# Kernel optimization log

Hardware: AMD Instinct MI355X
Metric: run time of the kernel (lower is better)

The kernel has to match this reference:

```python
import jax, jax.numpy as jnp
import numpy as np

HEADS = 16
DIM_HEAD = 64
SCALE = DIM_HEAD ** -0.5
MASK_VALUE = -jnp.finfo(jnp.float32).max


def setup_inputs() -> dict:
    key = jax.random.key(0)
    ks = jax.random.split(key, 6)
    b, n, dim = 2, 2048, 1024
    mem_len = 2048
    inner = HEADS * DIM_HEAD  # 1024
    return {
        "x": jax.random.normal(ks[0], (b, n, dim), jnp.float32),
        "mem_k": jax.random.normal(ks[1], (b, mem_len, inner), jnp.float32),
        "mem_v": jax.random.normal(ks[2], (b, mem_len, inner), jnp.float32),
        "pos_bias": jax.random.normal(ks[3], (HEADS, n, mem_len + n), jnp.float32) * 0.02,
        "Wq": jax.random.normal(ks[4], (dim, inner), jnp.float32) * (dim ** -0.5),
        "Wkv": jax.random.normal(ks[5], (dim, 2 * inner), jnp.float32) * (dim ** -0.5),
    }


def reference(x, mem_k, mem_v, pos_bias, Wq, Wkv):
    b, n, _ = x.shape
    # projections (note: original module returns before applying to_out)
    q = (x @ Wq) * SCALE                      # [b, n, h*d]
    k, v = jnp.split(x @ Wkv, 2, axis=-1)     # each [b, n, h*d]
    k = jnp.concatenate((mem_k, k), axis=1)   # [b, j, h*d]
    v = jnp.concatenate((mem_v, v), axis=1)

    def split_heads(t):
        return t.reshape(t.shape[0], t.shape[1], HEADS, DIM_HEAD).transpose(0, 2, 1, 3)

    q, k, v = map(split_heads, (q, k, v))     # [b, h, i/j, d]
    sim = jnp.einsum('bhid,bhjd->bhij', q, k)
    sim = sim + pos_bias[None]                # broadcast over batch
    i, j = sim.shape[-2:]
    # causal mask: triu with offset j - i + 1 is masked out
    causal_mask = jnp.triu(jnp.ones((i, j), dtype=bool), k=j - i + 1)
    sim = jnp.where(causal_mask[None, None], MASK_VALUE, sim)
    attn = jax.nn.softmax(sim, axis=-1)
    out = jnp.einsum('bhij,bhjd->bhid', attn, v)     # [b, h, i, d]
    out = out.transpose(0, 2, 1, 3).reshape(b, n, HEADS * DIM_HEAD)
    return out
```

## Files before the change

kernel.cpp:

```cpp
#include <hip/hip_runtime.h>
#include <hip/hip_bf16.h>
#include <cstdint>

#define B_     2
#define N_     2048
#define DIM_   1024
#define H_     16
#define DH_    64
#define MEM_   2048
#define JT_    4096
#define INNER_ 1024
#define SCALE_ 0.125f

typedef float f32x4 __attribute__((ext_vector_type(4)));
typedef short s16x8 __attribute__((ext_vector_type(8)));
typedef short s16x4 __attribute__((ext_vector_type(4)));

__device__ __forceinline__ short bf16_of(float f) {
    __hip_bfloat16 h = __float2bfloat16(f);
    return *(short*)&h;
}

__device__ __forceinline__ void gload16(const void* g, short* l) {
    __builtin_amdgcn_global_load_lds(
        (const __attribute__((address_space(1))) unsigned int*)g,
        (__attribute__((address_space(3))) unsigned int*)l, 16, 0, 0);
}

__global__ __launch_bounds__(256) void cast_x(
    const float* __restrict__ x, short* __restrict__ xb)
{
    const int total4 = B_ * N_ * DIM_ / 4;
    for (int idx = blockIdx.x * blockDim.x + threadIdx.x; idx < total4;
         idx += gridDim.x * blockDim.x) {
        float4 v = ((const float4*)x)[idx];
        s16x4 o;
        o[0] = bf16_of(v.x); o[1] = bf16_of(v.y);
        o[2] = bf16_of(v.z); o[3] = bf16_of(v.w);
        *(s16x4*)&xb[idx * 4] = o;
    }
}

__global__ __launch_bounds__(256) void cast_w(
    const float* __restrict__ Wq, const float* __restrict__ Wkv,
    short* __restrict__ Wt)
{
    const int kt = blockIdx.x;
    const int nt = blockIdx.y;
    __shared__ float tile[64][65];
    const int t = threadIdx.x;
    const int r = t >> 2, s4 = (t & 3) * 16;

    const int n0 = nt * 64;
    const float* src;
    int ldn, nc0;
    if (n0 < 1024) { src = Wq;  ldn = 1024; nc0 = n0; }
    else           { src = Wkv; ldn = 2048; nc0 = n0 - 1024; }
    const float scale = (n0 < 1024) ? SCALE_ : 1.0f;

#pragma unroll
    for (int kq = 0; kq < 4; ++kq) {
        float4 v = *(const float4*)&src[(size_t)(kt * 64 + r) * ldn + nc0 + s4 + kq * 4];
        tile[s4 + kq * 4 + 0][r] = v.x;
        tile[s4 + kq * 4 + 1][r] = v.y;
        tile[s4 + kq * 4 + 2][r] = v.z;
        tile[s4 + kq * 4 + 3][r] = v.w;
    }
    __syncthreads();
    short ov[16];
#pragma unroll
    for (int e = 0; e < 16; ++e) ov[e] = bf16_of(tile[r][s4 + e] * scale);
    short* dst = &Wt[(size_t)(n0 + r) * 1024 + kt * 64 + s4];
    *(s16x8*)&dst[0] = *(s16x8*)&ov[0];
    *(s16x8*)&dst[8] = *(s16x8*)&ov[8];
}

#define PLDC 152

__global__ __launch_bounds__(256) void mfma_proj(
    const short* __restrict__ Wt, const short* __restrict__ xb,
    short* __restrict__ qbuf, short* __restrict__ kbuf, short* __restrict__ vtbuf)
{
    const int bc = blockIdx.x;
    const int bi = blockIdx.y;
    const int tid = threadIdx.x;
    const int w = tid >> 6, lane = tid & 63, g = lane >> 4, li = lane & 15;
    const int wr = w >> 1, wc = w & 1;

    __shared__ short smem[128 * PLDC];
    short* A_lds = smem;
    short* B_lds = smem + 8192;

    f32x4 acc[4][4];
#pragma unroll
    for (int m = 0; m < 4; ++m)
#pragma unroll
        for (int n = 0; n < 4; ++n) acc[m][n] = f32x4{0.f, 0.f, 0.f, 0.f};

    const size_t arow0 = (size_t)bc * 128;
    const size_t brow0 = (size_t)bi * 128;

    for (int t = 0; t < 16; ++t) {
        __syncthreads();
#pragma unroll
        for (int u = 0; u < 4; ++u) {
            const int c = (w * 4 + u) * 64 + lane;
            const int row = c >> 3, q = c & 7;
            const int qs = q ^ (row & 7);
            gload16(&Wt[(arow0 + row) * 1024 + t * 64 + qs * 8],
                    &A_lds[(w * 4 + u) * 512 + lane * 8]);
            gload16(&xb[(brow0 + row) * 1024 + t * 64 + qs * 8],
                    &B_lds[(w * 4 + u) * 512 + lane * 8]);
        }
        __syncthreads();
#pragma unroll
        for (int kc = 0; kc < 2; ++kc) {
            s16x8 af[4], bf[4];
#pragma unroll
            for (int mt = 0; mt < 4; ++mt) {
                const int row = wr * 64 + mt * 16 + li;
                af[mt] = *(const s16x8*)&A_lds[row * 64 + ((kc * 4 + g) ^ (row & 7)) * 8];
            }
#pragma unroll
            for (int nt = 0; nt < 4; ++nt) {
                const int row = wc * 64 + nt * 16 + li;
                bf[nt] = *(const s16x8*)&B_lds[row * 64 + ((kc * 4 + g) ^ (row & 7)) * 8];
            }
#pragma unroll
            for (int mt = 0; mt < 4; ++mt)
#pragma unroll
                for (int nt = 0; nt < 4; ++nt)
                    acc[mt][nt] = __builtin_amdgcn_mfma_f32_16x16x32_bf16(af[mt], bf[nt], acc[mt][nt], 0, 0, 0);
        }
    }

    __syncthreads();
    const int c0 = bc * 128;
    const int i0g = bi * 128;
    const int b = i0g >> 11;
    const int ii0 = i0g & 2047;

    if (c0 < 2048) {
#pragma unroll
        for (int mt = 0; mt < 4; ++mt)
#pragma unroll
            for (int nt = 0; nt < 4; ++nt) {
                const int i_l = wc * 64 + nt * 16 + li;
                const int c_l = wr * 64 + mt * 16 + g * 4;
                s16x4 v4;
                v4[0] = bf16_of(acc[mt][nt][0]);
                v4[1] = bf16_of(acc[mt][nt][1]);
                v4[2] = bf16_of(acc[mt][nt][2]);
                v4[3] = bf16_of(acc[mt][nt][3]);
                *(s16x4*)&smem[i_l * PLDC + c_l] = v4;
            }
        __syncthreads();
        const bool isq = (c0 < 1024);
#pragma unroll
        for (int u = 0; u < 8; ++u) {
            const int ch = tid + u * 256;
            const int i_l = ch >> 4, seg = ch & 15;
            s16x8 v = *(const s16x8*)&smem[i_l * PLDC + seg * 8];
            const int cg = c0 + seg * 8;
            const int h = (cg >> 6) & 15;
            const int d = cg & 63;
            if (isq)
                *(s16x8*)&qbuf[(((size_t)(b * H_ + h)) * N_ + ii0 + i_l) * DH_ + d] = v;
            else
                *(s16x8*)&kbuf[(((size_t)(b * H_ + h)) * JT_ + MEM_ + ii0 + i_l) * DH_ + d] = v;
        }
    } else {
#pragma unroll
        for (int mt = 0; mt < 4; ++mt)
#pragma unroll
            for (int nt = 0; nt < 4; ++nt) {
                const int i_l = wc * 64 + nt * 16 + li;
                const int c_b = wr * 64 + mt * 16 + g * 4;
#pragma unroll
                for (int r = 0; r < 4; ++r)
                    smem[(c_b + r) * PLDC + i_l] = bf16_of(acc[mt][nt][r]);
            }
        __syncthreads();
#pragma unroll
        for (int u = 0; u < 8; ++u) {
            const int ch = tid + u * 256;
            const int c_l = ch >> 4, seg = ch & 15;
            s16x8 v = *(const s16x8*)&smem[c_l * PLDC + seg * 8];
            const int cv = c0 + c_l - 2048;
            const int h = cv >> 6, d = cv & 63;
            *(s16x8*)&vtbuf[(((size_t)(b * H_ + h)) * DH_ + d) * JT_ + MEM_ + ii0 + seg * 8] = v;
        }
    }
}

__global__ __launch_bounds__(256) void copymem_k(
    const float* __restrict__ mem_k, short* __restrict__ kbuf)
{
    const int total4 = B_ * MEM_ * INNER_ / 4;
    for (int idx = blockIdx.x * blockDim.x + threadIdx.x; idx < total4;
         idx += gridDim.x * blockDim.x) {
        const int flat = idx * 4;
        const int c = flat & 1023;
        const int j = (flat >> 10) & 2047;
        const int b = flat >> 21;
        const int h = c >> 6, d = c & 63;
        float4 v = ((const float4*)mem_k)[idx];
        s16x4 o;
        o[0] = bf16_of(v.x); o[1] = bf16_of(v.y);
        o[2] = bf16_of(v.z); o[3] = bf16_of(v.w);
        *(s16x4*)&kbuf[(((size_t)(b * H_ + h)) * JT_ + j) * DH_ + d] = o;
    }
}

__global__ __launch_bounds__(256) void transpose_memv(
    const float* __restrict__ mem_v, short* __restrict__ vtbuf)
{
    const int jt = blockIdx.x, h = blockIdx.y, b = blockIdx.z;
    const int j0 = jt * 64;
    __shared__ float tile[64][65];
    const int t = threadIdx.x;
    const int r = t >> 2, s4 = (t & 3) * 16;
#pragma unroll
    for (int k = 0; k < 4; ++k) {
        float4 v = *(const float4*)&mem_v[((size_t)(b * MEM_ + j0 + r)) * INNER_ + h * DH_ + s4 + k * 4];
        tile[s4 + k * 4 + 0][r] = v.x;
        tile[s4 + k * 4 + 1][r] = v.y;
        tile[s4 + k * 4 + 2][r] = v.z;
        tile[s4 + k * 4 + 3][r] = v.w;
    }
    __syncthreads();
    short ov[16];
#pragma unroll
    for (int e = 0; e < 16; ++e) ov[e] = bf16_of(tile[r][s4 + e]);
    short* dst = &vtbuf[((size_t)((b * H_ + h) * DH_ + r)) * JT_ + j0 + s4];
    *(s16x8*)&dst[0] = *(s16x8*)&ov[0];
    *(s16x8*)&dst[8] = *(s16x8*)&ov[8];
}

#define LPP 72

__global__ __launch_bounds__(512) void attn_flash(
    const short* __restrict__ qbuf, const short* __restrict__ kbuf,
    const short* __restrict__ vtbuf, const float* __restrict__ pos_bias,
    float* __restrict__ out)
{
    const int lid = blockIdx.x;
    const int k_  = lid & 255;
    const int hi  = lid >> 8;
    const int h   = (k_ & 7) | (((k_ >> 3) & 1) << 3);
    const int b   = (k_ >> 4) & 1;
    const int ztl = k_ >> 5;
    const int zt  = hi ? (15 - ztl) : ztl;
    const int i0  = zt * 128;

    const int tid = threadIdx.x;
    const int w = tid >> 6, lane = tid & 63, g = lane >> 4, li = lane & 15;

    __shared__ short K_lds[2][64 * 64];
    __shared__ short VT_lds[2][64 * 64];
    __shared__ short P_lds[8][16 * LPP];

    const size_t bh = (size_t)(b * H_ + h);
    const short* kg  = kbuf  + bh * (size_t)JT_ * DH_;
    const short* vtg = vtbuf + bh * (size_t)DH_ * JT_;
    const float* pb  = pos_bias + (size_t)h * N_ * JT_;

    const int qw = i0 + w * 16;

    s16x8 aq[2];
#pragma unroll
    for (int kc = 0; kc < 2; ++kc)
        aq[kc] = *(const s16x8*)&qbuf[(bh * N_ + qw + li) * DH_ + kc * 32 + g * 8];

    f32x4 o[4];
    float m_run = -3.0e38f, l_run = 0.f;
#pragma unroll
    for (int dt = 0; dt < 4; ++dt) o[dt] = f32x4{0.f, 0.f, 0.f, 0.f};

    const int ntiles = 34 + 2 * zt;

    #define STAGE(bufi, j0s)                                                   \
    {                                                                          \
        const int c = tid;                                                     \
        const int row = c >> 3, q = c & 7;                                     \
        const int qs = q ^ (row & 7);                                          \
        gload16(&kg[(size_t)((j0s) + row) * DH_ + qs * 8],                     \
                &K_lds[bufi][c * 8]);                                          \
        gload16(&vtg[(size_t)row * JT_ + (j0s) + qs * 8],                      \
                &VT_lds[bufi][c * 8]);                                         \
    }

    f32x4 bnext[4];
    #define LOADB(j0s)                                                         \
    {                                                                          \
        _Pragma("unroll")                                                      \
        for (int nt = 0; nt < 4; ++nt)                                         \
            bnext[nt] = *(const f32x4*)&pb[(size_t)(qw + li) * JT_ + (j0s) + nt * 16 + g * 4]; \
    }

    STAGE(0, 0);
    LOADB(0);
    __syncthreads();

    for (int t = 0; t < ntiles; ++t) {
        const int cur = t & 1;
        const int j0 = t * 64;
        const bool more = (t + 1 < ntiles);

        if (more) STAGE(cur ^ 1, j0 + 64);

        f32x4 sacc[4];
#pragma unroll
        for (int nt = 0; nt < 4; ++nt) sacc[nt] = bnext[nt];

        if (more) LOADB(j0 + 64);

        __builtin_amdgcn_s_setprio(1);
#pragma unroll
        for (int kc = 0; kc < 2; ++kc)
#pragma unroll
            for (int nt = 0; nt < 4; ++nt) {
                s16x8 bk = *(const s16x8*)&K_lds[cur][(nt * 16 + li) * 64 + ((kc * 4 + g) ^ (li & 7)) * 8];
                sacc[nt] = __builtin_amdgcn_mfma_f32_16x16x32_bf16(bk, aq[kc], sacc[nt], 0, 0, 0);
            }
        __builtin_amdgcn_s_setprio(0);

        const int q = qw + li;
        if (j0 + 63 > MEM_ + qw) {
#pragma unroll
            for (int nt = 0; nt < 4; ++nt)
#pragma unroll
                for (int r = 0; r < 4; ++r) {
                    const int jg = j0 + nt * 16 + g * 4 + r;
                    if (jg > MEM_ + q) sacc[nt][r] = -1e30f;
                }
        }

        float t0 = fmaxf(fmaxf(sacc[0][0], sacc[0][1]), fmaxf(sacc[0][2], sacc[0][3]));
        float t1 = fmaxf(fmaxf(sacc[1][0], sacc[1][1]), fmaxf(sacc[1][2], sacc[1][3]));
        float t2 = fmaxf(fmaxf(sacc[2][0], sacc[2][1]), fmaxf(sacc[2][2], sacc[2][3]));
        float t3 = fmaxf(fmaxf(sacc[3][0], sacc[3][1]), fmaxf(sacc[3][2], sacc[3][3]));
        float tm = fmaxf(fmaxf(t0, t1), fmaxf(t2, t3));
        tm = fmaxf(tm, __shfl_xor(tm, 16));
        tm = fmaxf(tm, __shfl_xor(tm, 32));
        const float m_new = fmaxf(m_run, tm);
        const float sc = __expf(m_run - m_new);
        m_run = m_new;

#pragma unroll
        for (int nt = 0; nt < 4; ++nt)
#pragma unroll
            for (int r = 0; r < 4; ++r)
                sacc[nt][r] = __expf(sacc[nt][r] - m_new);

        float s0 = (sacc[0][0] + sacc[0][1]) + (sacc[0][2] + sacc[0][3]);
        float s1 = (sacc[1][0] + sacc[1][1]) + (sacc[1][2] + sacc[1][3]);
        float s2 = (sacc[2][0] + sacc[2][1]) + (sacc[2][2] + sacc[2][3]);
        float s3 = (sacc[3][0] + sacc[3][1]) + (sacc[3][2] + sacc[3][3]);
        float ts = (s0 + s1) + (s2 + s3);
        ts += __shfl_xor(ts, 16);
        ts += __shfl_xor(ts, 32);
        l_run = l_run * sc + ts;
#pragma unroll
        for (int dt = 0; dt < 4; ++dt) o[dt] *= sc;

#pragma unroll
        for (int nt = 0; nt < 4; ++nt) {
            s16x4 pk;
            pk[0] = bf16_of(sacc[nt][0]);
            pk[1] = bf16_of(sacc[nt][1]);
            pk[2] = bf16_of(sacc[nt][2]);
            pk[3] = bf16_of(sacc[nt][3]);
            *(s16x4*)&P_lds[w][li * LPP + nt * 16 + g * 4] = pk;
        }

        __builtin_amdgcn_s_setprio(1);
#pragma unroll
        for (int kc = 0; kc < 2; ++kc) {
            s16x8 pf = *(const s16x8*)&P_lds[w][li * LPP + kc * 32 + g * 8];
#pragma unroll
            for (int dt = 0; dt < 4; ++dt) {
                s16x8 bv = *(const s16x8*)&VT_lds[cur][(dt * 16 + li) * 64 + ((kc * 4 + g) ^ (li & 7)) * 8];
                o[dt] = __builtin_amdgcn_mfma_f32_16x16x32_bf16(bv, pf, o[dt], 0, 0, 0);
            }
        }
        __builtin_amdgcn_s_setprio(0);

        __syncthreads();
    }
    #undef STAGE
    #undef LOADB

    {
        const float rinv = 1.0f / l_run;
        const int q = qw + li;
#pragma unroll
        for (int dt = 0; dt < 4; ++dt) {
            f32x4 ov = o[dt] * rinv;
            *(f32x4*)&out[((size_t)(b * N_ + q)) * INNER_ + h * DH_ + dt * 16 + g * 4] = ov;
        }
    }
}

extern "C" void kernel_launch(void* const* d_in, const int* in_sizes, int n_in,
                              void* d_out, int out_size, void* d_ws, size_t ws_size,
                              hipStream_t stream)
{
    const float* x        = (const float*)d_in[0];
    const float* mem_k    = (const float*)d_in[1];
    const float* mem_v    = (const float*)d_in[2];
    const float* pos_bias = (const float*)d_in[3];
    const float* Wq       = (const float*)d_in[4];
    const float* Wkv      = (const float*)d_in[5];
    float* out = (float*)d_out;

    char* ws = (char*)d_ws;
    short* qbuf  = (short*)(ws);
    short* kbuf  = (short*)(ws + (8u << 20));
    short* vtbuf = (short*)(ws + (24u << 20));
    short* xb    = (short*)(ws + (40u << 20));
    short* Wt    = (short*)(ws + (48u << 20));

    cast_x<<<2048, 256, 0, stream>>>(x, xb);
    cast_w<<<dim3(16, 48), 256, 0, stream>>>(Wq, Wkv, Wt);
    copymem_k<<<2048, 256, 0, stream>>>(mem_k, kbuf);
    transpose_memv<<<dim3(32, H_, B_), 256, 0, stream>>>(mem_v, vtbuf);

    mfma_proj<<<dim3(24, 32), 256, 0, stream>>>(Wt, xb, qbuf, kbuf, vtbuf);

    attn_flash<<<512, 512, 0, stream>>>(qbuf, kbuf, vtbuf, pos_bias, out);
}
```

Measured before the change: 238.7 us.

## Shrink attention blocks to 64 query rows, merge mem prep kernels, swizzle P tile

Result: faster. 228.0 us (-4.5%).

```diff
diff --git a/kernel.cpp b/kernel.cpp
--- a/kernel.cpp
+++ b/kernel.cpp
@@ -193,72 +193,69 @@
     }
 }
 
-__global__ __launch_bounds__(256) void copymem_k(
-    const float* __restrict__ mem_k, short* __restrict__ kbuf)
-{
-    const int total4 = B_ * MEM_ * INNER_ / 4;
-    for (int idx = blockIdx.x * blockDim.x + threadIdx.x; idx < total4;
-         idx += gridDim.x * blockDim.x) {
-        const int flat = idx * 4;
-        const int c = flat & 1023;
-        const int j = (flat >> 10) & 2047;
-        const int b = flat >> 21;
-        const int h = c >> 6, d = c & 63;
-        float4 v = ((const float4*)mem_k)[idx];
-        s16x4 o;
-        o[0] = bf16_of(v.x); o[1] = bf16_of(v.y);
-        o[2] = bf16_of(v.z); o[3] = bf16_of(v.w);
-        *(s16x4*)&kbuf[(((size_t)(b * H_ + h)) * JT_ + j) * DH_ + d] = o;
-    }
-}
-
-__global__ __launch_bounds__(256) void transpose_memv(
-    const float* __restrict__ mem_v, short* __restrict__ vtbuf)
-{
-    const int jt = blockIdx.x, h = blockIdx.y, b = blockIdx.z;
+__global__ __launch_bounds__(256) void prep_mem(
+    const float* __restrict__ mem_k, const float* __restrict__ mem_v,
+    short* __restrict__ kbuf, short* __restrict__ vtbuf)
+{
+    const int jt = blockIdx.x, h = blockIdx.y;
+    const int b = blockIdx.z & 1, task = blockIdx.z >> 1;
     const int j0 = jt * 64;
-    __shared__ float tile[64][65];
     const int t = threadIdx.x;
     const int r = t >> 2, s4 = (t & 3) * 16;
-#pragma unroll
-    for (int k = 0; k < 4; ++k) {
-        float4 v = *(const float4*)&mem_v[((size_t)(b * MEM_ + j0 + r)) * INNER_ + h * DH_ + s4 + k * 4];
-        tile[s4 + k * 4 + 0][r] = v.x;
-        tile[s4 + k * 4 + 1][r] = v.y;
-        tile[s4 + k * 4 + 2][r] = v.z;
-        tile[s4 + k * 4 + 3][r] = v.w;
-    }
-    __syncthreads();
-    short ov[16];
-#pragma unroll
-    for (int e = 0; e < 16; ++e) ov[e] = bf16_of(tile[r][s4 + e]);
-    short* dst = &vtbuf[((size_t)((b * H_ + h) * DH_ + r)) * JT_ + j0 + s4];
-    *(s16x8*)&dst[0] = *(s16x8*)&ov[0];
-    *(s16x8*)&dst[8] = *(s16x8*)&ov[8];
-}
-
-#define LPP 72
-
-__global__ __launch_bounds__(512) void attn_flash(
+    const size_t bh = (size_t)(b * H_ + h);
+
+    if (task == 0) {
+        short ov[16];
+#pragma unroll
+        for (int k = 0; k < 4; ++k) {
+            float4 v = *(const float4*)&mem_k[((size_t)(b * MEM_ + j0 + r)) * INNER_ + h * DH_ + s4 + k * 4];
+            ov[k * 4 + 0] = bf16_of(v.x);
+            ov[k * 4 + 1] = bf16_of(v.y);
+            ov[k * 4 + 2] = bf16_of(v.z);
+            ov[k * 4 + 3] = bf16_of(v.w);
+        }
+        short* dst = &kbuf[(bh * JT_ + j0 + r) * DH_ + s4];
+        *(s16x8*)&dst[0] = *(s16x8*)&ov[0];
+        *(s16x8*)&dst[8] = *(s16x8*)&ov[8];
+    } else {
+        __shared__ float tile[64][65];
+#pragma unroll
+        for (int k = 0; k < 4; ++k) {
+            float4 v = *(const float4*)&mem_v[((size_t)(b * MEM_ + j0 + r)) * INNER_ + h * DH_ + s4 + k * 4];
+            tile[s4 + k * 4 + 0][r] = v.x;
+            tile[s4 + k * 4 + 1][r] = v.y;
+            tile[s4 + k * 4 + 2][r] = v.z;
+            tile[s4 + k * 4 + 3][r] = v.w;
+        }
+        __syncthreads();
+        short ov[16];
+#pragma unroll
+        for (int e = 0; e < 16; ++e) ov[e] = bf16_of(tile[r][s4 + e]);
+        short* dst = &vtbuf[(bh * DH_ + r) * JT_ + j0 + s4];
+        *(s16x8*)&dst[0] = *(s16x8*)&ov[0];
+        *(s16x8*)&dst[8] = *(s16x8*)&ov[8];
+    }
+}
+
+__global__ __launch_bounds__(256, 4) void attn_flash(
     const short* __restrict__ qbuf, const short* __restrict__ kbuf,
     const short* __restrict__ vtbuf, const float* __restrict__ pos_bias,
     float* __restrict__ out)
 {
     const int lid = blockIdx.x;
-    const int k_  = lid & 255;
-    const int hi  = lid >> 8;
-    const int h   = (k_ & 7) | (((k_ >> 3) & 1) << 3);
-    const int b   = (k_ >> 4) & 1;
-    const int ztl = k_ >> 5;
-    const int zt  = hi ? (15 - ztl) : ztl;
-    const int i0  = zt * 128;
+    const int h   = (lid & 7) | (((lid >> 3) & 1) << 3);
+    const int b   = (lid >> 4) & 1;
+    const int zql = (lid >> 5) & 15;
+    const int hi  = lid >> 9;
+    const int zq  = hi ? (31 - zql) : zql;
+    const int i0  = zq * 64;
 
     const int tid = threadIdx.x;
     const int w = tid >> 6, lane = tid & 63, g = lane >> 4, li = lane & 15;
 
     __shared__ short K_lds[2][64 * 64];
     __shared__ short VT_lds[2][64 * 64];
-    __shared__ short P_lds[8][16 * LPP];
+    __shared__ short P_lds[4][16 * 64];
 
     const size_t bh = (size_t)(b * H_ + h);
     const short* kg  = kbuf  + bh * (size_t)JT_ * DH_;
@@ -277,17 +274,20 @@
 #pragma unroll
     for (int dt = 0; dt < 4; ++dt) o[dt] = f32x4{0.f, 0.f, 0.f, 0.f};
 
-    const int ntiles = 34 + 2 * zt;
+    const int ntiles = 33 + zq;
 
     #define STAGE(bufi, j0s)                                                   \
     {                                                                          \
-        const int c = tid;                                                     \
-        const int row = c >> 3, q = c & 7;                                     \
-        const int qs = q ^ (row & 7);                                          \
-        gload16(&kg[(size_t)((j0s) + row) * DH_ + qs * 8],                     \
-                &K_lds[bufi][c * 8]);                                          \
-        gload16(&vtg[(size_t)row * JT_ + (j0s) + qs * 8],                      \
-                &VT_lds[bufi][c * 8]);                                         \
+        _Pragma("unroll")                                                      \
+        for (int u = 0; u < 2; ++u) {                                          \
+            const int c = u * 256 + tid;                                       \
+            const int row = c >> 3, q = c & 7;                                 \
+            const int qs = q ^ (row & 7);                                      \
+            gload16(&kg[(size_t)((j0s) + row) * DH_ + qs * 8],                 \
+                    &K_lds[bufi][c * 8]);                                      \
+            gload16(&vtg[(size_t)row * JT_ + (j0s) + qs * 8],                  \
+                    &VT_lds[bufi][c * 8]);                                     \
+        }                                                                      \
     }
 
     f32x4 bnext[4];
@@ -366,18 +366,21 @@
 
 #pragma unroll
         for (int nt = 0; nt < 4; ++nt) {
+            const int sl = nt * 4 + g;
+            const int gi = (sl >> 1) ^ (li & 7);
             s16x4 pk;
             pk[0] = bf16_of(sacc[nt][0]);
             pk[1] = bf16_of(sacc[nt][1]);
             pk[2] = bf16_of(sacc[nt][2]);
             pk[3] = bf16_of(sacc[nt][3]);
-            *(s16x4*)&P_lds[w][li * LPP + nt * 16 + g * 4] = pk;
+            *(s16x4*)&P_lds[w][li * 64 + gi * 8 + (sl & 1) * 4] = pk;
         }
 
         __builtin_amdgcn_s_setprio(1);
 #pragma unroll
         for (int kc = 0; kc < 2; ++kc) {
-            s16x8 pf = *(const s16x8*)&P_lds[w][li * LPP + kc * 32 + g * 8];
+            const int gir = (kc * 4 + g) ^ (li & 7);
+            s16x8 pf = *(const s16x8*)&P_lds[w][li * 64 + gir * 8];
 #pragma unroll
             for (int dt = 0; dt < 4; ++dt) {
                 s16x8 bv = *(const s16x8*)&VT_lds[cur][(dt * 16 + li) * 64 + ((kc * 4 + g) ^ (li & 7)) * 8];
@@ -423,10 +426,9 @@
 
     cast_x<<<2048, 256, 0, stream>>>(x, xb);
     cast_w<<<dim3(16, 48), 256, 0, stream>>>(Wq, Wkv, Wt);
-    copymem_k<<<2048, 256, 0, stream>>>(mem_k, kbuf);
-    transpose_memv<<<dim3(32, H_, B_), 256, 0, stream>>>(mem_v, vtbuf);
+    prep_mem<<<dim3(32, H_, 4), 256, 0, stream>>>(mem_k, mem_v, kbuf, vtbuf);
 
     mfma_proj<<<dim3(24, 32), 256, 0, stream>>>(Wt, xb, qbuf, kbuf, vtbuf);
 
-    attn_flash<<<512, 512, 0, stream>>>(qbuf, kbuf, vtbuf, pos_bias, out);
-}
+    attn_flash<<<1024, 256, 0, stream>>>(qbuf, kbuf, vtbuf, pos_bias, out);
+}
```
